# Optimization experiments

Measured on AMD Instinct MI355X. Metric: run time of the kernel, lower is better.

Reference implementation:

```python
import jax, jax.numpy as jnp
import numpy as np

H = 300  # hidden_size

def _u(key, shape):
    return jax.random.uniform(key, shape, minval=-0.1, maxval=0.1, dtype=jnp.float32)

def setup_inputs() -> dict:
    key = jax.random.key(0)
    ks = jax.random.split(key, 20)
    B, T = 128, 64
    return {
        "local_inputs": jax.random.normal(ks[0], (B, T, 20, 12), dtype=jnp.float32),
        "labels": jax.random.normal(ks[1], (B, T, 1, 1), dtype=jnp.float32),
        "extras": jax.random.normal(ks[2], (B, T, 17, 1), dtype=jnp.float32),
        "DisM": jax.random.uniform(ks[3], (12,), dtype=jnp.float32),
        "AngleM": jax.random.uniform(ks[4], (12,), dtype=jnp.float32),
        # 12 neighbor LSTMCells (input 8 -> hidden 300); W_hh omitted since h0=0
        "W_ih": _u(ks[5], (12, 4 * H, 8)),
        "b_ih": _u(ks[6], (12, 4 * H)),
        "b_hh": _u(ks[7], (12, 4 * H)),
        # target LSTMCell (input 5 -> hidden 300)
        "Wt_ih": _u(ks[8], (4 * H, 5)),
        "bt_ih": _u(ks[9], (4 * H,)),
        "bt_hh": _u(ks[10], (4 * H,)),
        "Att1": _u(ks[11], (600, 200)),
        "ba1": _u(ks[12], (200,)),
        "Att2": _u(ks[13], (202, 1)),
        "ba2": _u(ks[14], (1,)),
        "fuse2": _u(ks[15], (600, 200)),
        "biasf2": _u(ks[16], (200,)),
        "Wout": _u(ks[17], (200, 1)),
        "biasout": _u(ks[18], (1,)),
    }

def _lstm_zero_state(gates):
    # PyTorch LSTMCell gate order i,f,g,o; zero initial (h, c):
    # c' = sigmoid(i)*tanh(g), h' = sigmoid(o)*tanh(c')
    i, f, g, o = jnp.split(gates, 4, axis=-1)
    c = jax.nn.sigmoid(i) * jnp.tanh(g)
    return jax.nn.sigmoid(o) * jnp.tanh(c)

def reference(local_inputs, labels, extras, DisM, AngleM,
              W_ih, b_ih, b_hh, Wt_ih, bt_ih, bt_hh,
              Att1, ba1, Att2, ba2, fuse2, biasf2, Wout, biasout):
    B, T = local_inputs.shape[0], local_inputs.shape[1]
    # Every LSTMCell is called with zero state each timestep -> no recurrence;
    # vectorize over all timesteps and the 12 neighbor channels at once.
    S = local_inputs[:, :, 0:8, :]                                 # [B,T,8,12]
    gates = jnp.einsum('btfc,cgf->btcg', S, W_ih) + b_ih + b_hh    # [B,T,12,1200]
    h = _lstm_zero_state(gates)                                    # [B,T,12,300]
    tgt = extras[:, :, 0:5, 0]                                     # [B,T,5]
    gt = jnp.einsum('btf,gf->btg', tgt, Wt_ih) + bt_ih + bt_hh     # [B,T,1200]
    htarget = _lstm_zero_state(gt)                                 # [B,T,300]
    # attention: per channel, relu(cat[htarget,h_i] @ Att1 + ba1), append wij rows 7,6
    ht12 = jnp.broadcast_to(htarget[:, :, None, :], (B, T, 12, H))
    cat = jnp.concatenate([ht12, h], axis=-1)                      # [B,T,12,600]
    a = jax.nn.relu(jnp.einsum('btcd,de->btce', cat, Att1) + ba1)  # [B,T,12,200]
    wij = jnp.stack([local_inputs[:, :, 7, :], local_inputs[:, :, 6, :]], axis=-1)  # [B,T,12,2]
    fc = jnp.concatenate([a, wij], axis=-1)                        # [B,T,12,202]
    score = jax.nn.relu(jnp.einsum('btcd,do->btco', fc, Att2) + ba2)[..., 0]  # [B,T,12]
    # faithful to source: scores detached (.tolist), softmax over the 12 channels
    # with layout [12,B], then RAW row-major reshape to [B,12] (not a transpose)
    st = jnp.transpose(score, (1, 2, 0))                           # [T,12,B]
    w = jax.nn.softmax(jax.lax.stop_gradient(st), axis=1)          # [T,12,B]
    w = w.reshape(T, B, 12)                                        # raw reshape as in torch
    w = jnp.transpose(w, (1, 0, 2))                                # [B,T,12]
    con = jnp.transpose(h, (0, 1, 3, 2))                           # [B,T,300,12]
    fusion = jnp.sum(con * w[:, :, None, :], axis=-1)              # [B,T,300]
    fusion = jnp.concatenate([fusion, htarget], axis=-1)           # [B,T,600]
    fuse = jnp.einsum('btd,de->bte', fusion, fuse2) + biasf2       # [B,T,200]
    predict = jnp.einsum('btd,do->bto', fuse, Wout) + biasout      # [B,T,1]
    predicts = jnp.transpose(predict, (1, 0, 2))                   # [T,B,1] (list over timesteps)
    labels_out = jnp.transpose(labels[:, :, 0, :], (1, 0, 2))      # [T,B,1]
    return predicts, labels_out
```

## Files before the change

### kernel.cpp

```cpp
#include <hip/hip_runtime.h>
#include <hip/hip_bf16.h>

#define HH   300
#define NB   128
#define NTT  64
#define NP   8192
#define NCH  12
#define KPAD 320
#define NTI2 14

typedef __attribute__((ext_vector_type(8))) short short8;
typedef __attribute__((ext_vector_type(4))) float f32x4;

__device__ __forceinline__ float fsig(float x){
  return __builtin_amdgcn_rcpf(1.f + __expf(-x));
}
__device__ __forceinline__ float ftanh(float x){
  float e = __expf(2.f*x);
  return 1.f - 2.f*__builtin_amdgcn_rcpf(e + 1.f);
}
__device__ __forceinline__ float bf2f(unsigned short u){
  return __uint_as_float(((unsigned)u) << 16);
}
__device__ __forceinline__ unsigned short f2bf(float f){
  __hip_bfloat16 h = __float2bfloat16(f);
  return *reinterpret_cast<unsigned short*>(&h);
}
__device__ __forceinline__ unsigned short rbf(float f){
  return (unsigned short)((__float_as_uint(f) + 0x8000u) >> 16);
}
__device__ __forceinline__ int swzi(int row, int col, int strideShorts){
  int byte = row*(strideShorts*2) + (col<<1);
  byte ^= (row & 7) << 4;
  return byte >> 1;
}

__global__ __launch_bounds__(256) void k_prep(
    const float* __restrict__ Att1, const float* __restrict__ ba1,
    const float* __restrict__ Wih, const float* __restrict__ bih,
    const float* __restrict__ bhh, const float* __restrict__ fuse2,
    const float* __restrict__ bf2, const float* __restrict__ Wout,
    const float* __restrict__ bout, const float* __restrict__ li,
    unsigned short* __restrict__ a1hi2, unsigned short* __restrict__ a1lo2,
    unsigned short* __restrict__ wg3, float* __restrict__ bsum3,
    unsigned short* __restrict__ Sbf, float* __restrict__ kconst)
{
  int bid = blockIdx.x, tid = threadIdx.x;
  if (bid == 1989){
    __shared__ float red[256];
    red[tid] = (tid < 200) ? bf2[tid]*Wout[tid] : 0.f;
    __syncthreads();
    for (int s=128; s>0; s>>=1){
      if (tid < s) red[tid] += red[tid+s];
      __syncthreads();
    }
    if (tid == 0) kconst[0] = red[0] + bout[0];
    return;
  }
  if (bid >= 965){
    int pb0 = (bid - 965) * 8;
    __shared__ float s_li[8*240];
    for (int i = tid; i < 8*240; i += 256)
      s_li[i] = li[(size_t)pb0*240 + i];
    __syncthreads();
    for (int i = tid; i < 8*96; i += 256){
      int pp = i / 96, rem = i - pp*96;
      int c = rem >> 3, f = rem & 7;
      Sbf[((size_t)c*NP + pb0 + pp)*8 + f] = f2bf(s_li[pp*240 + f*12 + c]);
    }
    return;
  }
  int id = bid*256 + tid;
  if (id < 71680){
    int e = id/320, k = id - e*320;
    float v = 0.f;
    if (e < 200 && k < 300){
      v = Att1[(size_t)(300+k)*200 + e];
    } else if (e == 208 && k < 300){
      const float* fr = fuse2 + (size_t)k*200;
      float a = 0.f;
      #pragma unroll 4
      for (int e2=0; e2<200; e2++) a += fr[e2]*Wout[e2];
      v = a;
    }
    a1hi2[id] = f2bf(v);
  } else if (id < 143360){
    int j = id - 71680;
    int e = j/320, k = j - e*320;
    float v = 0.f;
    if (e < 200){
      if (k < 300)       v = Att1[(size_t)k*200 + e];
      else if (k == 300) v = ba1[e];
    } else if (e == 208 && k < 300){
      const float* fr = fuse2 + (size_t)(300+k)*200;
      float a = 0.f;
      #pragma unroll 4
      for (int e2=0; e2<200; e2++) a += fr[e2]*Wout[e2];
      v = a;
    }
    a1lo2[j] = f2bf(v);
  } else if (id < 235520){
    int idx = id - 143360;
    int c = idx / 7680, rem = idx - c*7680;
    int np = rem >> 3, f = rem & 7;
    int G = np / 320, j = np - G*320;
    int off = (G==0) ? 0 : (G==1) ? 600 : 900;
    float v = (j<300) ? Wih[(size_t)c*9600 + (size_t)(off+j)*8 + f] : 0.f;
    wg3[idx] = f2bf(v);
  } else {
    int idx = id - 235520;
    int c = idx / 960, np = idx - c*960;
    int G = np / 320, j = np - G*320;
    int off = (G==0) ? 0 : (G==1) ? 600 : 900;
    bsum3[idx] = (j<300) ? (bih[c*1200+off+j] + bhh[c*1200+off+j]) : 0.f;
  }
}

#define PB 32
__global__ __launch_bounds__(320) void k_ht(
    const float* __restrict__ extras, const float* __restrict__ Wt,
    const float* __restrict__ bti, const float* __restrict__ bth,
    const unsigned short* __restrict__ a1lo2,
    float* __restrict__ ta, float* __restrict__ Tbuf)
{
  int p0 = blockIdx.x * PB;
  int tid = threadIdx.x;
  __shared__ __align__(16) unsigned short s_ht[PB*KPAD];
  __shared__ float s_e[PB][5];
  if (tid < PB*5) s_e[tid/5][tid%5] = extras[(size_t)(p0 + tid/5)*17 + (tid%5)];
  __syncthreads();

  int j = tid;
  if (j < 300){
    float w[15];
    #pragma unroll
    for (int f=0; f<5; f++){
      w[f]    = Wt[(size_t)j*5 + f];
      w[5+f]  = Wt[(size_t)(j+600)*5 + f];
      w[10+f] = Wt[(size_t)(j+900)*5 + f];
    }
    float bi = bti[j]     + bth[j];
    float bg = bti[j+600] + bth[j+600];
    float bo = bti[j+900] + bth[j+900];
    for (int pp=0; pp<PB; pp++){
      float gi=bi, gg=bg, go=bo;
      #pragma unroll
      for (int f=0; f<5; f++){
        float t = s_e[pp][f];
        gi += t*w[f]; gg += t*w[5+f]; go += t*w[10+f];
      }
      float cc = fsig(gi)*ftanh(gg);
      s_ht[swzi(pp, j, KPAD)] = rbf(fsig(go)*ftanh(cc));
    }
  } else {
    unsigned short v = (j == 300) ? (unsigned short)0x3F80 : (unsigned short)0;
    for (int pp=0; pp<PB; pp++)
      s_ht[swzi(pp, j, KPAD)] = v;
  }
  __syncthreads();

  int wave = tid >> 6, lane = tid & 63;
  int lr = lane & 15, lg = lane >> 4;
  f32x4 acc[2][3];
  #pragma unroll
  for (int mt=0; mt<2; mt++)
    #pragma unroll
    for (int t=0; t<3; t++) acc[mt][t] = (f32x4){0.f,0.f,0.f,0.f};
  for (int k0=0; k0<KPAD; k0+=32){
    short8 a[2];
    #pragma unroll
    for (int mt=0; mt<2; mt++)
      a[mt] = *(const short8*)&s_ht[swzi(mt*16 + lr, lg*8 + k0, KPAD)];
    #pragma unroll
    for (int t=0; t<3; t++){
      int nt = wave + t*5;
      if (nt < NTI2){
        short8 b = *(const short8*)(a1lo2 + (size_t)(nt*16 + lr)*KPAD + lg*8 + k0);
        #pragma unroll
        for (int mt=0; mt<2; mt++)
          acc[mt][t] = __builtin_amdgcn_mfma_f32_16x16x32_bf16(a[mt], b, acc[mt][t], 0, 0, 0);
      }
    }
  }
  #pragma unroll
  for (int t=0; t<3; t++){
    int nt = wave + t*5;
    if (nt < 13){
      int e = nt*16 + lr;
      if (e < 200){
        #pragma unroll
        for (int mt=0; mt<2; mt++)
          #pragma unroll
          for (int i=0; i<4; i++)
            ta[(size_t)(p0 + mt*16 + lg*4 + i)*200 + e] = acc[mt][t][i];
      }
    } else if (nt == 13 && lr == 0){
      #pragma unroll
      for (int mt=0; mt<2; mt++)
        #pragma unroll
        for (int i=0; i<4; i++)
          Tbuf[p0 + mt*16 + lg*4 + i] = acc[mt][t][i];
    }
  }
}

__global__ __launch_bounds__(256, 4) void k_hs(
    const float* __restrict__ li, const unsigned short* __restrict__ Sbf,
    const unsigned short* __restrict__ wg3, const float* __restrict__ bsum3,
    const unsigned short* __restrict__ a1hi2, const float* __restrict__ ta,
    const float* __restrict__ att2, const float* __restrict__ ba2,
    float* __restrict__ Hbuf, float* __restrict__ score)
{
  int c  = blockIdx.x >> 7;
  int p0 = (blockIdx.x & 127) << 6;
  int tid = threadIdx.x;
  int wave = tid >> 6, lane = tid & 63;
  int lr = lane & 15, lg = lane >> 4;
  __shared__ __align__(16) unsigned short s_h[64*KPAD];

  short8 z8 = (short8){0,0,0,0,0,0,0,0};
  short8 afrag = z8;
  if (lg == 0)
    afrag = *(const short8*)(Sbf + ((size_t)c*NP + p0 + wave*16 + lr)*8);

  const unsigned short* wgc = wg3 + (size_t)c*960*8;
  const float* bsc = bsum3 + (size_t)c*960;
  f32x4 zero4 = (f32x4){0.f,0.f,0.f,0.f};
  int rowb = wave*16 + lg*4;
  short8 nb0 = z8, nb1 = z8, nb2 = z8;
  if (lg == 0){
    nb0 = *(const short8*)&wgc[(size_t)(      lr)*8];
    nb1 = *(const short8*)&wgc[(size_t)(320 + lr)*8];
    nb2 = *(const short8*)&wgc[(size_t)(640 + lr)*8];
  }
  for (int ch = 0; ch < 20; ch++){
    int n0 = ch*16;
    short8 cb0 = nb0, cb1 = nb1, cb2 = nb2;
    if (ch < 19 && lg == 0){
      int nn = n0 + 16 + lr;
      nb0 = *(const short8*)&wgc[(size_t)(      nn)*8];
      nb1 = *(const short8*)&wgc[(size_t)(320 + nn)*8];
      nb2 = *(const short8*)&wgc[(size_t)(640 + nn)*8];
    }
    f32x4 gi4 = __builtin_amdgcn_mfma_f32_16x16x32_bf16(afrag, cb0, zero4, 0, 0, 0);
    f32x4 gg4 = __builtin_amdgcn_mfma_f32_16x16x32_bf16(afrag, cb1, zero4, 0, 0, 0);
    f32x4 go4 = __builtin_amdgcn_mfma_f32_16x16x32_bf16(afrag, cb2, zero4, 0, 0, 0);
    float bi = bsc[      n0 + lr];
    float bg = bsc[320 + n0 + lr];
    float bo = bsc[640 + n0 + lr];
    #pragma unroll
    for (int i2=0; i2<4; i2++){
      float gi = gi4[i2] + bi;
      float gg = gg4[i2] + bg;
      float go = go4[i2] + bo;
      float cc = fsig(gi)*ftanh(gg);
      float hv = fsig(go)*ftanh(cc);
      s_h[swzi(rowb + i2, n0 + lr, KPAD)] = rbf(hv);
    }
  }
  __syncthreads();

  f32x4 acc[4][4];
  #pragma unroll
  for (int mt=0; mt<4; mt++)
    #pragma unroll
    for (int t4=0; t4<4; t4++) acc[mt][t4] = zero4;
  for (int k0=0; k0<KPAD; k0+=32){
    short8 a[4];
    #pragma unroll
    for (int mt=0; mt<4; mt++)
      a[mt] = *(const short8*)&s_h[swzi(mt*16 + lr, lg*8 + k0, KPAD)];
    #pragma unroll
    for (int t4=0; t4<4; t4++){
      int nt = wave + t4*4;
      if (nt < NTI2){
        short8 b = *(const short8*)(a1hi2 + (size_t)(nt*16 + lr)*KPAD + lg*8 + k0);
        #pragma unroll
        for (int mt=0; mt<4; mt++)
          acc[mt][t4] = __builtin_amdgcn_mfma_f32_16x16x32_bf16(a[mt], b, acc[mt][t4], 0, 0, 0);
      }
    }
  }

  float sacc[4][4];
  #pragma unroll
  for (int mt=0; mt<4; mt++)
    #pragma unroll
    for (int i=0; i<4; i++) sacc[mt][i] = 0.f;
  #pragma unroll
  for (int t4=0; t4<4; t4++){
    int nt = wave + t4*4;
    if (nt < 13){
      int e = nt*16 + lr;
      if (e < 200){
        float a2v = att2[e];
        #pragma unroll
        for (int mt=0; mt<4; mt++){
          #pragma unroll
          for (int i=0; i<4; i++){
            int p = p0 + mt*16 + lg*4 + i;
            float v = acc[mt][t4][i] + ta[(size_t)p*200 + e];
            sacc[mt][i] += fmaxf(v, 0.f) * a2v;
          }
        }
      }
    } else if (nt == 13 && lr == 0){
      #pragma unroll
      for (int mt=0; mt<4; mt++)
        #pragma unroll
        for (int i=0; i<4; i++)
          Hbuf[(size_t)(p0 + mt*16 + lg*4 + i)*NCH + c] = acc[mt][t4][i];
    }
  }
  __syncthreads();
  float* s_red = reinterpret_cast<float*>(s_h);
  #pragma unroll
  for (int mt=0; mt<4; mt++){
    #pragma unroll
    for (int i=0; i<4; i++){
      float s = sacc[mt][i];
      s += __shfl_xor(s, 1);
      s += __shfl_xor(s, 2);
      s += __shfl_xor(s, 4);
      s += __shfl_xor(s, 8);
      if (lr == 0) s_red[wave*64 + mt*16 + lg*4 + i] = s;
    }
  }
  __syncthreads();
  if (tid < 64){
    float r = s_red[tid] + s_red[64+tid] + s_red[128+tid] + s_red[192+tid];
    int p = p0 + tid;
    float w200 = att2[200], w201 = att2[201], b2 = ba2[0];
    float w0 = li[(size_t)p*240 + 84 + c];
    float w1 = li[(size_t)p*240 + 72 + c];
    score[(size_t)p*NCH + c] = fmaxf(r + w0*w200 + w1*w201 + b2, 0.f);
  }
}

__global__ __launch_bounds__(128) void k_sm_final(
    const float* __restrict__ score, const float* __restrict__ Hbuf,
    const float* __restrict__ Tbuf, const float* __restrict__ kconst,
    const float* __restrict__ labels, float* __restrict__ out)
{
  int t = blockIdx.x;
  int b = threadIdx.x;
  __shared__ float ws_f[NCH*NB];
  int p = b*NTT + t;
  const float* s = score + (size_t)p*NCH;
  float v[NCH];
  float m = -1e30f;
  #pragma unroll
  for (int c=0; c<NCH; c++){ v[c] = s[c]; m = fmaxf(m, v[c]); }
  float sum = 0.f;
  #pragma unroll
  for (int c=0; c<NCH; c++){ v[c] = __expf(v[c]-m); sum += v[c]; }
  float inv = __builtin_amdgcn_rcpf(sum);
  #pragma unroll
  for (int c=0; c<NCH; c++)
    ws_f[c*NB + b] = v[c]*inv;
  __syncthreads();
  float acc = Tbuf[p] + kconst[0];
  const float* Hp = Hbuf + (size_t)p*NCH;
  int base = b*NCH;
  #pragma unroll
  for (int c=0; c<NCH; c++)
    acc += ws_f[base + c] * Hp[c];
  out[(size_t)t*NB + b] = acc;
  out[NP + (size_t)t*NB + b] = labels[p];
}

extern "C" void kernel_launch(void* const* d_in, const int* in_sizes, int n_in,
                              void* d_out, int out_size, void* d_ws, size_t ws_size,
                              hipStream_t stream)
{
  const float* li     = (const float*)d_in[0];
  const float* labels = (const float*)d_in[1];
  const float* extras = (const float*)d_in[2];
  const float* Wih    = (const float*)d_in[5];
  const float* bih    = (const float*)d_in[6];
  const float* bhh    = (const float*)d_in[7];
  const float* Wt     = (const float*)d_in[8];
  const float* bti    = (const float*)d_in[9];
  const float* bth    = (const float*)d_in[10];
  const float* Att1   = (const float*)d_in[11];
  const float* ba1    = (const float*)d_in[12];
  const float* Att2   = (const float*)d_in[13];
  const float* ba2    = (const float*)d_in[14];
  const float* fuse2  = (const float*)d_in[15];
  const float* bf2    = (const float*)d_in[16];
  const float* Wout   = (const float*)d_in[17];
  const float* bout   = (const float*)d_in[18];
  float* out = (float*)d_out;

  char* ws = (char*)d_ws;
  float* ta     = (float*)ws;
  float* score  = (float*)(ws + 6553600);
  float* Hbuf   = (float*)(ws + 6946816);
  float* Tbuf   = (float*)(ws + 7340032);
  unsigned short* a1hi2 = (unsigned short*)(ws + 7372800);
  unsigned short* a1lo2 = (unsigned short*)(ws + 7516160);
  unsigned short* wg3   = (unsigned short*)(ws + 7659520);
  float* bsum3  = (float*)(ws + 7843840);
  unsigned short* Sbf   = (unsigned short*)(ws + 7889920);
  float* kconst = (float*)(ws + 9462784);

  k_prep<<<1990, 256, 0, stream>>>(Att1, ba1, Wih, bih, bhh, fuse2, bf2,
                                   Wout, bout, li,
                                   a1hi2, a1lo2, wg3, bsum3, Sbf, kconst);
  k_ht<<<NP/PB, 320, 0, stream>>>(extras, Wt, bti, bth, a1lo2, ta, Tbuf);
  k_hs<<<NCH*128, 256, 0, stream>>>(li, Sbf, wg3, bsum3, a1hi2, ta, Att2, ba2,
                                    Hbuf, score);
  k_sm_final<<<NTT, NB, 0, stream>>>(score, Hbuf, Tbuf, kconst, labels, out);
}
```

Before: 190.2 us.

## Halve k_hs row tile to 32 and split gate work across waves; vectorize prep dot

k_hs now processes 32 positions per block instead of 64 and launches twice as many blocks. In the LSTM stage the four waves split the 20 gate column chunks into two halves of 10 across two row groups, dropping the software-prefetched weight loads. The score GEMM keeps half as many accumulators. This targets more blocks, more occupancy and shorter per-block serial gate work, at the cost of reading the a1hi2 weights twice as often. Separately, the fuse2·Wout dot in k_prep is vectorized with float4 loads, four partial sums and Wout staged in shared memory.

```diff
diff --git a/kernel.cpp b/kernel.cpp
--- a/kernel.cpp
+++ b/kernel.cpp
@@ -70,6 +70,9 @@
     }
     return;
   }
+  __shared__ float s_wout[200];
+  for (int i = tid; i < 200; i += 256) s_wout[i] = Wout[i];
+  __syncthreads();
   int id = bid*256 + tid;
   if (id < 71680){
     int e = id/320, k = id - e*320;
@@ -77,11 +80,15 @@
     if (e < 200 && k < 300){
       v = Att1[(size_t)(300+k)*200 + e];
     } else if (e == 208 && k < 300){
-      const float* fr = fuse2 + (size_t)k*200;
-      float a = 0.f;
-      #pragma unroll 4
-      for (int e2=0; e2<200; e2++) a += fr[e2]*Wout[e2];
-      v = a;
+      const float4* fr4 = (const float4*)(fuse2 + (size_t)k*200);
+      float a0=0.f,a1=0.f,a2=0.f,a3=0.f;
+      #pragma unroll 5
+      for (int q=0; q<50; q++){
+        float4 f = fr4[q];
+        float4 w = *(const float4*)&s_wout[q*4];
+        a0 += f.x*w.x; a1 += f.y*w.y; a2 += f.z*w.z; a3 += f.w*w.w;
+      }
+      v = (a0+a1)+(a2+a3);
     }
     a1hi2[id] = f2bf(v);
   } else if (id < 143360){
@@ -92,11 +99,15 @@
       if (k < 300)       v = Att1[(size_t)k*200 + e];
       else if (k == 300) v = ba1[e];
     } else if (e == 208 && k < 300){
-      const float* fr = fuse2 + (size_t)(300+k)*200;
-      float a = 0.f;
-      #pragma unroll 4
-      for (int e2=0; e2<200; e2++) a += fr[e2]*Wout[e2];
-      v = a;
+      const float4* fr4 = (const float4*)(fuse2 + (size_t)(300+k)*200);
+      float a0=0.f,a1=0.f,a2=0.f,a3=0.f;
+      #pragma unroll 5
+      for (int q=0; q<50; q++){
+        float4 f = fr4[q];
+        float4 w = *(const float4*)&s_wout[q*4];
+        a0 += f.x*w.x; a1 += f.y*w.y; a2 += f.z*w.z; a3 += f.w*w.w;
+      }
+      v = (a0+a1)+(a2+a3);
     }
     a1lo2[j] = f2bf(v);
   } else if (id < 235520){
@@ -204,43 +215,39 @@
   }
 }
 
-__global__ __launch_bounds__(256, 4) void k_hs(
+#define PB2 32
+__global__ __launch_bounds__(256) void k_hs(
     const float* __restrict__ li, const unsigned short* __restrict__ Sbf,
     const unsigned short* __restrict__ wg3, const float* __restrict__ bsum3,
     const unsigned short* __restrict__ a1hi2, const float* __restrict__ ta,
     const float* __restrict__ att2, const float* __restrict__ ba2,
     float* __restrict__ Hbuf, float* __restrict__ score)
 {
-  int c  = blockIdx.x >> 7;
-  int p0 = (blockIdx.x & 127) << 6;
+  int c  = blockIdx.x >> 8;
+  int p0 = (blockIdx.x & 255) << 5;
   int tid = threadIdx.x;
   int wave = tid >> 6, lane = tid & 63;
   int lr = lane & 15, lg = lane >> 4;
-  __shared__ __align__(16) unsigned short s_h[64*KPAD];
+  __shared__ __align__(16) unsigned short s_h[PB2*KPAD];
 
   short8 z8 = (short8){0,0,0,0,0,0,0,0};
+  int rg  = wave & 1;
+  int chb = (wave >> 1) * 10;
   short8 afrag = z8;
   if (lg == 0)
-    afrag = *(const short8*)(Sbf + ((size_t)c*NP + p0 + wave*16 + lr)*8);
+    afrag = *(const short8*)(Sbf + ((size_t)c*NP + p0 + rg*16 + lr)*8);
 
   const unsigned short* wgc = wg3 + (size_t)c*960*8;
   const float* bsc = bsum3 + (size_t)c*960;
   f32x4 zero4 = (f32x4){0.f,0.f,0.f,0.f};
-  int rowb = wave*16 + lg*4;
-  short8 nb0 = z8, nb1 = z8, nb2 = z8;
-  if (lg == 0){
-    nb0 = *(const short8*)&wgc[(size_t)(      lr)*8];
-    nb1 = *(const short8*)&wgc[(size_t)(320 + lr)*8];
-    nb2 = *(const short8*)&wgc[(size_t)(640 + lr)*8];
-  }
-  for (int ch = 0; ch < 20; ch++){
-    int n0 = ch*16;
-    short8 cb0 = nb0, cb1 = nb1, cb2 = nb2;
-    if (ch < 19 && lg == 0){
-      int nn = n0 + 16 + lr;
-      nb0 = *(const short8*)&wgc[(size_t)(      nn)*8];
-      nb1 = *(const short8*)&wgc[(size_t)(320 + nn)*8];
-      nb2 = *(const short8*)&wgc[(size_t)(640 + nn)*8];
+  int rowb = rg*16 + lg*4;
+  for (int ch = 0; ch < 10; ch++){
+    int n0 = (chb + ch)*16;
+    short8 cb0 = z8, cb1 = z8, cb2 = z8;
+    if (lg == 0){
+      cb0 = *(const short8*)&wgc[(size_t)(      n0 + lr)*8];
+      cb1 = *(const short8*)&wgc[(size_t)(320 + n0 + lr)*8];
+      cb2 = *(const short8*)&wgc[(size_t)(640 + n0 + lr)*8];
     }
     f32x4 gi4 = __builtin_amdgcn_mfma_f32_16x16x32_bf16(afrag, cb0, zero4, 0, 0, 0);
     f32x4 gg4 = __builtin_amdgcn_mfma_f32_16x16x32_bf16(afrag, cb1, zero4, 0, 0, 0);
@@ -260,15 +267,15 @@
   }
   __syncthreads();
 
-  f32x4 acc[4][4];
-  #pragma unroll
-  for (int mt=0; mt<4; mt++)
+  f32x4 acc[2][4];
+  #pragma unroll
+  for (int mt=0; mt<2; mt++)
     #pragma unroll
     for (int t4=0; t4<4; t4++) acc[mt][t4] = zero4;
   for (int k0=0; k0<KPAD; k0+=32){
-    short8 a[4];
-    #pragma unroll
-    for (int mt=0; mt<4; mt++)
+    short8 a[2];
+    #pragma unroll
+    for (int mt=0; mt<2; mt++)
       a[mt] = *(const short8*)&s_h[swzi(mt*16 + lr, lg*8 + k0, KPAD)];
     #pragma unroll
     for (int t4=0; t4<4; t4++){
@@ -276,15 +283,15 @@
       if (nt < NTI2){
         short8 b = *(const short8*)(a1hi2 + (size_t)(nt*16 + lr)*KPAD + lg*8 + k0);
         #pragma unroll
-        for (int mt=0; mt<4; mt++)
+        for (int mt=0; mt<2; mt++)
           acc[mt][t4] = __builtin_amdgcn_mfma_f32_16x16x32_bf16(a[mt], b, acc[mt][t4], 0, 0, 0);
       }
     }
   }
 
-  float sacc[4][4];
-  #pragma unroll
-  for (int mt=0; mt<4; mt++)
+  float sacc[2][4];
+  #pragma unroll
+  for (int mt=0; mt<2; mt++)
     #pragma unroll
     for (int i=0; i<4; i++) sacc[mt][i] = 0.f;
   #pragma unroll
@@ -295,7 +302,7 @@
       if (e < 200){
         float a2v = att2[e];
         #pragma unroll
-        for (int mt=0; mt<4; mt++){
+        for (int mt=0; mt<2; mt++){
           #pragma unroll
           for (int i=0; i<4; i++){
             int p = p0 + mt*16 + lg*4 + i;
@@ -306,7 +313,7 @@
       }
     } else if (nt == 13 && lr == 0){
       #pragma unroll
-      for (int mt=0; mt<4; mt++)
+      for (int mt=0; mt<2; mt++)
         #pragma unroll
         for (int i=0; i<4; i++)
           Hbuf[(size_t)(p0 + mt*16 + lg*4 + i)*NCH + c] = acc[mt][t4][i];
@@ -315,7 +322,7 @@
   __syncthreads();
   float* s_red = reinterpret_cast<float*>(s_h);
   #pragma unroll
-  for (int mt=0; mt<4; mt++){
+  for (int mt=0; mt<2; mt++){
     #pragma unroll
     for (int i=0; i<4; i++){
       float s = sacc[mt][i];
@@ -323,12 +330,12 @@
       s += __shfl_xor(s, 2);
       s += __shfl_xor(s, 4);
       s += __shfl_xor(s, 8);
-      if (lr == 0) s_red[wave*64 + mt*16 + lg*4 + i] = s;
-    }
-  }
-  __syncthreads();
-  if (tid < 64){
-    float r = s_red[tid] + s_red[64+tid] + s_red[128+tid] + s_red[192+tid];
+      if (lr == 0) s_red[wave*32 + mt*16 + lg*4 + i] = s;
+    }
+  }
+  __syncthreads();
+  if (tid < 32){
+    float r = s_red[tid] + s_red[32+tid] + s_red[64+tid] + s_red[96+tid];
     int p = p0 + tid;
     float w200 = att2[200], w201 = att2[201], b2 = ba2[0];
     float w0 = li[(size_t)p*240 + 84 + c];
@@ -408,7 +415,7 @@
                                    Wout, bout, li,
                                    a1hi2, a1lo2, wg3, bsum3, Sbf, kconst);
   k_ht<<<NP/PB, 320, 0, stream>>>(extras, Wt, bti, bth, a1lo2, ta, Tbuf);
-  k_hs<<<NCH*128, 256, 0, stream>>>(li, Sbf, wg3, bsum3, a1hi2, ta, Att2, ba2,
+  k_hs<<<NCH*256, 256, 0, stream>>>(li, Sbf, wg3, bsum3, a1hi2, ta, Att2, ba2,
                                     Hbuf, score);
   k_sm_final<<<NTT, NB, 0, stream>>>(score, Hbuf, Tbuf, kconst, labels, out);
 }
```

Measured after the change: 198.9 us. +4.5%, slower.
